# Performance work log

Hardware: AMD Instinct MI355X
Metric: run time of the kernel (lower is better)

## Reference

```python
import jax, jax.numpy as jnp
import numpy as np

NUM_EMBEDDINGS = 1024
EMBEDDING_DIM = 64
COMMITMENT_COST = 0.25


def setup_inputs() -> dict:
    key = jax.random.key(0)
    k1, k2 = jax.random.split(key)
    z_e = jax.random.normal(k1, (32, EMBEDDING_DIM, 32, 32), dtype=jnp.float32)
    # codebook init: uniform(-1/K, 1/K) as in the torch module
    embedding = jax.random.uniform(
        k2, (NUM_EMBEDDINGS, EMBEDDING_DIM), dtype=jnp.float32,
        minval=-1.0 / NUM_EMBEDDINGS, maxval=1.0 / NUM_EMBEDDINGS)
    return {"z_e": z_e, "embedding": embedding}


def reference(z_e, embedding):
    B, C, H, W = z_e.shape
    # (B,C,H,W) -> (B,H,W,C) -> (N,C)
    z = jnp.transpose(z_e, (0, 2, 3, 1))
    z_flat = z.reshape(-1, C)
    # squared L2 distances: |z|^2 - 2 z e^T + |e|^2  -> (N, K)
    distances = (jnp.sum(z_flat ** 2, axis=1, keepdims=True)
                 - 2.0 * z_flat @ embedding.T
                 + jnp.sum(embedding ** 2, axis=1))
    encoding_indices = jnp.argmin(distances, axis=1)  # (N,)
    z_q = embedding[encoding_indices].reshape(z.shape)  # (B,H,W,C)
    # use_ema=True branch: loss = commitment_cost * mse(z, sg(z_q))
    commitment_loss = jnp.mean((z - jax.lax.stop_gradient(z_q)) ** 2)
    loss = COMMITMENT_COST * commitment_loss
    # straight-through estimator
    z_q_ste = z + jax.lax.stop_gradient(z_q - z)
    z_q_ste = jnp.transpose(z_q_ste, (0, 3, 1, 2))  # back to (B,C,H,W)
    indices = encoding_indices.reshape(B, H, W)
    return z_q_ste, loss, indices
```

## Files before the change

kernel.cpp:

```cpp
#include <hip/hip_runtime.h>
#include <hip/hip_bf16.h>
#include <math.h>
#include <stdint.h>

#define NUM_EMB 1024
#define DIM 64
#define LOSS_OFF 2097152
#define IDX_OFF 2097153
#define NROWS 32768
#define CAND_CAP 1024

typedef float f32x4 __attribute__((ext_vector_type(4)));
typedef short bf16x8 __attribute__((ext_vector_type(8)));

__device__ __forceinline__ float np_fold16(float* y) {
#pragma unroll
    for (int j = 0; j < 8; ++j) y[j] = __fadd_rn(y[j], y[j + 8]);
#pragma unroll
    for (int j = 0; j < 4; ++j) y[j] = __fadd_rn(y[j], y[j + 4]);
    y[0] = __fadd_rn(y[0], y[2]);
    y[1] = __fadd_rn(y[1], y[3]);
    return __fadd_rn(y[0], y[1]);
}

__device__ __forceinline__ unsigned short bf16bits(float f) {
    __hip_bfloat16 h = __float2bfloat16(f);
    return *reinterpret_cast<unsigned short*>(&h);
}

__global__ void vq_emb_norms(const float* __restrict__ emb,
                             float* __restrict__ norms,
                             float* __restrict__ out) {
    int k = blockIdx.x * blockDim.x + threadIdx.x;
    if (k == 0) out[LOSS_OFF] = 0.0f;
    if (k < NUM_EMB) {
        const float4* e4 = reinterpret_cast<const float4*>(emb + k * DIM);
        float e2[DIM];
#pragma unroll
        for (int q = 0; q < 16; ++q) {
            const float4 v = e4[q];
            e2[q * 4 + 0] = v.x; e2[q * 4 + 1] = v.y;
            e2[q * 4 + 2] = v.z; e2[q * 4 + 3] = v.w;
        }
        float y[16];
#pragma unroll
        for (int j = 0; j < 16; ++j) {
            float a = __fadd_rn(__fmul_rn(e2[j],      e2[j]),
                                __fmul_rn(e2[j + 16], e2[j + 16]));
            float b = __fadd_rn(__fmul_rn(e2[j + 32], e2[j + 32]),
                                __fmul_rn(e2[j + 48], e2[j + 48]));
            y[j] = __fadd_rn(a, b);
        }
        norms[k] = np_fold16(y);
    }
}

__device__ inline unsigned long long exact_key(
        const float* __restrict__ z_e, const float* __restrict__ emb,
        const float* __restrict__ norms, long zrowbase, int k) {
    float z[DIM];
#pragma unroll
    for (int c = 0; c < DIM; ++c) z[c] = z_e[zrowbase + (long)c * 1024];
    float A;
    {
        float y[16];
#pragma unroll
        for (int j = 0; j < 16; ++j) {
            float a  = __fadd_rn(__fmul_rn(z[j],      z[j]),
                                 __fmul_rn(z[j + 16], z[j + 16]));
            float c2 = __fadd_rn(__fmul_rn(z[j + 32], z[j + 32]),
                                 __fmul_rn(z[j + 48], z[j + 48]));
            y[j] = __fadd_rn(a, c2);
        }
        A = np_fold16(y);
    }
    const float4* ep = reinterpret_cast<const float4*>(emb + (size_t)k * DIM);
    float dot = 0.f;
#pragma unroll
    for (int q = 0; q < 16; ++q) {
        const float4 e4 = ep[q];
        dot = __fmaf_rn(z[4 * q + 0], e4.x, dot);
        dot = __fmaf_rn(z[4 * q + 1], e4.y, dot);
        dot = __fmaf_rn(z[4 * q + 2], e4.z, dot);
        dot = __fmaf_rn(z[4 * q + 3], e4.w, dot);
    }
    const float d = __fadd_rn(__fmaf_rn(-2.f, dot, A), norms[k]);
    return ((unsigned long long)__float_as_uint(d) << 32) | (unsigned)k;
}

__device__ __forceinline__ void stage_ebf(short* s_ebf,
                                          const float* __restrict__ emb,
                                          int ch, int tid) {
#pragma unroll
    for (int it = 0; it < 8; ++it) {
        const int idx = it * 512 + tid;
        const int cl  = idx >> 4;
        const int cq  = idx & 15;
        const float4 v = *reinterpret_cast<const float4*>(
            emb + (size_t)(ch * 256 + cl) * 64 + 4 * cq);
        uint2 pk;
        pk.x = (unsigned)bf16bits(v.x) | ((unsigned)bf16bits(v.y) << 16);
        pk.y = (unsigned)bf16bits(v.z) | ((unsigned)bf16bits(v.w) << 16);
        const int byte = cl * 128 + ((8 * cq) ^ ((cl & 7) << 4));
        *reinterpret_cast<uint2*>(reinterpret_cast<char*>(s_ebf) + byte) = pk;
    }
}

__device__ __forceinline__ f32x4 tile_dot(const short* s_ebf, int cl, int kb,
                                          bf16x8 a0, bf16x8 a1) {
    const char* base = reinterpret_cast<const char*>(s_ebf) + cl * 128;
    const int sw = (cl & 7) << 4;
    const bf16x8 b0 = *reinterpret_cast<const bf16x8*>(base + ((16 * kb) ^ sw));
    const bf16x8 b1 = *reinterpret_cast<const bf16x8*>(base + ((64 + 16 * kb) ^ sw));
    f32x4 C = {0.f, 0.f, 0.f, 0.f};
    C = __builtin_amdgcn_mfma_f32_16x16x32_bf16(a0, b0, C, 0, 0, 0);
    C = __builtin_amdgcn_mfma_f32_16x16x32_bf16(a1, b1, C, 0, 0, 0);
    return C;
}

__global__ __launch_bounds__(512, 4)
void vq_mfma_fused(const float* __restrict__ z_e,
                   const float* __restrict__ emb,
                   const float* __restrict__ norms,
                   float* __restrict__ out) {
    __shared__ short s_zbf[64 * 64];
    __shared__ short s_ebf[256 * 64];
    __shared__ float s_pmin[2][64];
    __shared__ float s_S[64];
    __shared__ unsigned int s_cand[CAND_CAP];
    __shared__ int s_cnt;
    __shared__ unsigned long long s_key[64];
    __shared__ int s_final[64];
    __shared__ float s_loss[8];

    const int tid  = threadIdx.x;
    const int lane = tid & 63;
    const int wave = __builtin_amdgcn_readfirstlane(tid >> 6);
    const int rt    = wave & 3;
    const int chalf = wave >> 2;

    const int n0  = blockIdx.x * 64;
    const int b   = n0 >> 10;
    const int hw0 = n0 & 1023;

    if (tid == 0) s_cnt = 0;
    if (tid < 64) s_key[tid] = ~0ull;

#pragma unroll
    for (int it = 0; it < 4; ++it) {
        const int idx = it * 512 + tid;
        const int hw  = idx & 63;
        const int cp  = idx >> 6;
        const float f0 = z_e[(long)b * 65536 + (long)(2 * cp)     * 1024 + hw0 + hw];
        const float f1 = z_e[(long)b * 65536 + (long)(2 * cp + 1) * 1024 + hw0 + hw];
        const unsigned int pk =
            (unsigned int)bf16bits(f0) | ((unsigned int)bf16bits(f1) << 16);
        const int byte = hw * 128 + ((4 * cp) ^ ((hw & 7) << 4));
        *reinterpret_cast<unsigned int*>(
            reinterpret_cast<char*>(s_zbf) + byte) = pk;
    }
    __syncthreads();

    const int rowA = rt * 16 + (lane & 15);
    const int kb   = lane >> 4;
    bf16x8 a0, a1;
    {
        const char* base = reinterpret_cast<const char*>(s_zbf) + rowA * 128;
        const int sw = (rowA & 7) << 4;
        a0 = *reinterpret_cast<const bf16x8*>(base + ((16 * kb) ^ sw));
        a1 = *reinterpret_cast<const bf16x8*>(base + ((64 + 16 * kb) ^ sw));
    }
    if (chalf == 0) {
        float s = 0.f;
#pragma unroll
        for (int j = 0; j < 8; ++j) {
            s += fabsf(__uint_as_float(((unsigned)(unsigned short)a0[j]) << 16));
            s += fabsf(__uint_as_float(((unsigned)(unsigned short)a1[j]) << 16));
        }
        s += __shfl_xor(s, 16, 64);
        s += __shfl_xor(s, 32, 64);
        if (kb == 0) s_S[rowA] = s;
    }

    float bestv[4] = {INFINITY, INFINITY, INFINITY, INFINITY};
    float secv[4]  = {INFINITY, INFINITY, INFINITY, INFINITY};
    int   bestc[4] = {0, 0, 0, 0};

    for (int ch = 0; ch < 4; ++ch) {
        __syncthreads();
        stage_ebf(s_ebf, emb, ch, tid);
        __syncthreads();
#pragma unroll
        for (int tt = 0; tt < 8; ++tt) {
            const int t    = chalf * 8 + tt;
            const int cl   = t * 16 + (lane & 15);
            const int code = ch * 256 + cl;
            const f32x4 C  = tile_dot(s_ebf, cl, kb, a0, a1);
            const float Ek = norms[code];
#pragma unroll
            for (int r = 0; r < 4; ++r) {
                const float v = __fmaf_rn(-2.f, C[r], Ek);
                if (v < bestv[r]) {
                    secv[r]  = bestv[r];
                    bestv[r] = v;  bestc[r] = code;
                } else if (v < secv[r]) {
                    secv[r] = v;
                }
            }
        }
    }

#pragma unroll
    for (int r = 0; r < 4; ++r) {
        float m = bestv[r];
        m = fminf(m, __shfl_xor(m, 1, 64));
        m = fminf(m, __shfl_xor(m, 2, 64));
        m = fminf(m, __shfl_xor(m, 4, 64));
        m = fminf(m, __shfl_xor(m, 8, 64));
        if ((lane & 15) == 0)
            s_pmin[chalf][rt * 16 + (lane >> 4) * 4 + r] = m;
    }
    __syncthreads();

#pragma unroll
    for (int r = 0; r < 4; ++r) {
        const int row = rt * 16 + (lane >> 4) * 4 + r;
        const float rowmin = fminf(s_pmin[0][row], s_pmin[1][row]);
        const float thr = rowmin + (3.0517578125e-5f * s_S[row] + 2e-4f);
        if (secv[r] <= thr) {
            for (int ch = 0; ch < 4; ++ch)
#pragma unroll
                for (int tt = 0; tt < 8; ++tt) {
                    const int code =
                        ch * 256 + (chalf * 8 + tt) * 16 + (lane & 15);
                    const int slot = atomicAdd(&s_cnt, 1);
                    if (slot < CAND_CAP)
                        s_cand[slot] = ((unsigned)row << 10) | (unsigned)code;
                }
        } else if (bestv[r] <= thr) {
            const int slot = atomicAdd(&s_cnt, 1);
            if (slot < CAND_CAP)
                s_cand[slot] = ((unsigned)row << 10) | (unsigned)bestc[r];
        }
    }
    __syncthreads();

    const int cnt = s_cnt;
    if (cnt <= CAND_CAP) {
        for (int i = tid; i < cnt; i += 512) {
            const unsigned int e = s_cand[i];
            const int row = (int)(e >> 10);
            const int k   = (int)(e & 1023u);
            const unsigned long long key =
                exact_key(z_e, emb, norms, (long)b * 65536 + hw0 + row, k);
            atomicMin(&s_key[row], key);
        }
    } else {
        for (int j = tid; j < 64 * 1024; j += 512) {
            const int row = j >> 10;
            const int k   = j & 1023;
            const unsigned long long key =
                exact_key(z_e, emb, norms, (long)b * 65536 + hw0 + row, k);
            atomicMin(&s_key[row], key);
        }
    }
    __syncthreads();

    if (tid < 64) {
        const int k = (int)(s_key[tid] & 0xFFFFFFFFull);
        s_final[tid] = k;
        out[IDX_OFF + n0 + tid] = (float)k;
    }
    __syncthreads();

    const long zbase = (long)b * 65536 + hw0 + lane;
    const int fidx = s_final[lane];
    float lsum = 0.f;
#pragma unroll
    for (int j = 0; j < DIM / 8; ++j) {
        const int c = wave * 8 + j;
        const float zc = z_e[zbase + (long)c * 1024];
        const float ec = emb[fidx * DIM + c];
        out[((long)(b * 64 + c)) * 1024 + hw0 + lane] = zc + (ec - zc);
        const float dlt = zc - ec;
        lsum = __fmaf_rn(dlt, dlt, lsum);
    }
#pragma unroll
    for (int off = 32; off >= 1; off >>= 1) lsum += __shfl_xor(lsum, off, 64);
    if (lane == 0) s_loss[wave] = lsum;
    __syncthreads();

    if (tid == 0) {
        float t = 0.f;
#pragma unroll
        for (int w = 0; w < 8; ++w) t = __fadd_rn(t, s_loss[w]);
        atomicAdd(out + LOSS_OFF, t * 1.1920928955078125e-07f);
    }
}

extern "C" void kernel_launch(void* const* d_in, const int* in_sizes, int n_in,
                              void* d_out, int out_size, void* d_ws, size_t ws_size,
                              hipStream_t stream) {
    const float* z_e = (const float*)d_in[0];
    const float* emb = (const float*)d_in[1];
    float* out   = (float*)d_out;
    float* norms = (float*)d_ws;

    vq_emb_norms<<<dim3(16), dim3(64), 0, stream>>>(emb, norms, out);
    vq_mfma_fused<<<dim3(NROWS / 64), dim3(512), 0, stream>>>(z_e, emb, norms, out);
}
```

Measured before the change: 99.62 us.

## Double-buffer codebook staging with register prefetch of next chunk

Codebook staging into LDS now uses two 128-code buffers instead of one 256-code buffer. The global load for chunk ch+2 is issued into registers while chunk ch+1 is written, so global latency overlaps with MFMA work. The aim is to hide the load latency that each chunk previously paid in full between barriers. The cost is twice as many chunks and barrier pairs, plus 16 extra registers per thread for the prefetch, which may pressure occupancy under the 512x4 launch bounds.

```diff
diff --git a/kernel.cpp b/kernel.cpp
--- a/kernel.cpp
+++ b/kernel.cpp
@@ -88,21 +88,26 @@
     return ((unsigned long long)__float_as_uint(d) << 32) | (unsigned)k;
 }
 
-__device__ __forceinline__ void stage_ebf(short* s_ebf,
-                                          const float* __restrict__ emb,
-                                          int ch, int tid) {
-#pragma unroll
-    for (int it = 0; it < 8; ++it) {
+__device__ __forceinline__ void ebf_load(const float4* __restrict__ emb4,
+                                         int ch, int tid, float4 pf[4]) {
+#pragma unroll
+    for (int it = 0; it < 4; ++it) {
+        const int idx = it * 512 + tid;
+        pf[it] = emb4[(size_t)(ch * 128 + (idx >> 4)) * 16 + (idx & 15)];
+    }
+}
+__device__ __forceinline__ void ebf_write(short* buf, int tid,
+                                          const float4 pf[4]) {
+#pragma unroll
+    for (int it = 0; it < 4; ++it) {
         const int idx = it * 512 + tid;
         const int cl  = idx >> 4;
         const int cq  = idx & 15;
-        const float4 v = *reinterpret_cast<const float4*>(
-            emb + (size_t)(ch * 256 + cl) * 64 + 4 * cq);
         uint2 pk;
-        pk.x = (unsigned)bf16bits(v.x) | ((unsigned)bf16bits(v.y) << 16);
-        pk.y = (unsigned)bf16bits(v.z) | ((unsigned)bf16bits(v.w) << 16);
+        pk.x = (unsigned)bf16bits(pf[it].x) | ((unsigned)bf16bits(pf[it].y) << 16);
+        pk.y = (unsigned)bf16bits(pf[it].z) | ((unsigned)bf16bits(pf[it].w) << 16);
         const int byte = cl * 128 + ((8 * cq) ^ ((cl & 7) << 4));
-        *reinterpret_cast<uint2*>(reinterpret_cast<char*>(s_ebf) + byte) = pk;
+        *reinterpret_cast<uint2*>(reinterpret_cast<char*>(buf) + byte) = pk;
     }
 }
 
@@ -124,7 +129,7 @@
                    const float* __restrict__ norms,
                    float* __restrict__ out) {
     __shared__ short s_zbf[64 * 64];
-    __shared__ short s_ebf[256 * 64];
+    __shared__ short s_ebf[2][128 * 64];
     __shared__ float s_pmin[2][64];
     __shared__ float s_S[64];
     __shared__ unsigned int s_cand[CAND_CAP];
@@ -145,6 +150,10 @@
 
     if (tid == 0) s_cnt = 0;
     if (tid < 64) s_key[tid] = ~0ull;
+
+    const float4* emb4 = reinterpret_cast<const float4*>(emb);
+    float4 pf[4];
+    ebf_load(emb4, 0, tid, pf);
 
 #pragma unroll
     for (int it = 0; it < 4; ++it) {
@@ -159,6 +168,8 @@
         *reinterpret_cast<unsigned int*>(
             reinterpret_cast<char*>(s_zbf) + byte) = pk;
     }
+    ebf_write(s_ebf[0], tid, pf);
+    ebf_load(emb4, 1, tid, pf);
     __syncthreads();
 
     const int rowA = rt * 16 + (lane & 15);
@@ -186,16 +197,14 @@
     float secv[4]  = {INFINITY, INFINITY, INFINITY, INFINITY};
     int   bestc[4] = {0, 0, 0, 0};
 
-    for (int ch = 0; ch < 4; ++ch) {
-        __syncthreads();
-        stage_ebf(s_ebf, emb, ch, tid);
-        __syncthreads();
-#pragma unroll
-        for (int tt = 0; tt < 8; ++tt) {
-            const int t    = chalf * 8 + tt;
+    for (int ch = 0; ch < 8; ++ch) {
+        const short* buf = s_ebf[ch & 1];
+#pragma unroll
+        for (int tt = 0; tt < 4; ++tt) {
+            const int t    = chalf * 4 + tt;
             const int cl   = t * 16 + (lane & 15);
-            const int code = ch * 256 + cl;
-            const f32x4 C  = tile_dot(s_ebf, cl, kb, a0, a1);
+            const int code = ch * 128 + cl;
+            const f32x4 C  = tile_dot(buf, cl, kb, a0, a1);
             const float Ek = norms[code];
 #pragma unroll
             for (int r = 0; r < 4; ++r) {
@@ -208,6 +217,12 @@
                 }
             }
         }
+        if (ch < 7) {
+            __syncthreads();
+            ebf_write(s_ebf[(ch + 1) & 1], tid, pf);
+            if (ch < 6) ebf_load(emb4, ch + 2, tid, pf);
+            __syncthreads();
+        }
     }
 
 #pragma unroll
@@ -228,11 +243,11 @@
         const float rowmin = fminf(s_pmin[0][row], s_pmin[1][row]);
         const float thr = rowmin + (3.0517578125e-5f * s_S[row] + 2e-4f);
         if (secv[r] <= thr) {
-            for (int ch = 0; ch < 4; ++ch)
-#pragma unroll
-                for (int tt = 0; tt < 8; ++tt) {
+            for (int ch = 0; ch < 8; ++ch)
+#pragma unroll
+                for (int tt = 0; tt < 4; ++tt) {
                     const int code =
-                        ch * 256 + (chalf * 8 + tt) * 16 + (lane & 15);
+                        ch * 128 + (chalf * 4 + tt) * 16 + (lane & 15);
                     const int slot = atomicAdd(&s_cnt, 1);
                     if (slot < CAND_CAP)
                         s_cand[slot] = ((unsigned)row << 10) | (unsigned)code;
```

New measurement: 99.52 us. Within noise of the previous version (-0.1%).
